# Kernel tuning notes

Measured on AMD Instinct MI355X. Metric: run time of the kernel, lower is better.

The kernel has to match this reference:

```python
import jax, jax.numpy as jnp
import numpy as np

L, N, E, H = 2048, 4, 2048, 16
D = E // H  # head_dim = 128
SCALE = D ** -0.5
NEG = -10000.0


def setup_inputs() -> dict:
    key = jax.random.key(0)
    ks = jax.random.split(key, 10)
    s = 0.02
    return {
        "query": jax.random.normal(ks[0], (L, N, E), jnp.float32),
        "key": jax.random.normal(ks[1], (L, N, E), jnp.float32),
        "wq": jax.random.normal(ks[2], (E, E), jnp.float32) * s,
        "wq_bias": jax.random.normal(ks[3], (E,), jnp.float32) * s,
        "wk": jax.random.normal(ks[4], (E, E), jnp.float32) * s,
        "wk_bias": jax.random.normal(ks[5], (E,), jnp.float32) * s,
        "wv": jax.random.normal(ks[6], (E, E), jnp.float32) * s,
        "wv_bias": jax.random.normal(ks[7], (E,), jnp.float32) * s,
        "wout": jax.random.normal(ks[8], (E, E), jnp.float32) * s,
        "wout_bias": jax.random.normal(ks[9], (E,), jnp.float32) * s,
    }


def reference(query, key, wq, wq_bias, wk, wk_bias, wv, wv_bias, wout, wout_bias):
    # query/key: (L, N, E). Projections: y = x @ W^T + b  (W: [inner, E])
    q = query @ wq.T + wq_bias          # (L, N, E)
    k = key @ wk.T + wk_bias
    v = key @ wv.T + wv_bias
    # split heads -> (N, H, L, D)
    def split(x):
        return x.reshape(L, N, H, D).transpose(1, 2, 0, 3)
    q, k, v = split(q) * SCALE, split(k), split(v)
    # scores (N, H, L, L) with causal mask (tril), fill -10000 like torch code
    attn = jnp.einsum("nhqd,nhkd->nhqk", q, k)
    causal = jnp.tril(jnp.ones((L, L), dtype=bool))
    attn = jnp.where(causal[None, None], attn, NEG)
    attn = jax.nn.softmax(attn, axis=-1)
    out = jnp.einsum("nhqk,nhkd->nhqd", attn, v)  # (N, H, L, D)
    out = out.transpose(2, 0, 1, 3).reshape(L, N, E)
    return out @ wout.T + wout_bias
```

## Files before the change

kernel.cpp:

```cpp
#include <hip/hip_runtime.h>
#include <hip/hip_bf16.h>
#include <cstdint>
#include <cstddef>

typedef __attribute__((ext_vector_type(8))) short short8;
typedef __attribute__((ext_vector_type(4))) float float4v;

#define L_SEQ 2048
#define N_B   4
#define E_DIM 2048
#define N_H   16
#define H_D   128
#define C1_SCALE_LOG2E 0.12751744f

static __device__ __forceinline__ unsigned short f2bf(float f) {
  union { float f; unsigned int u; } x; x.f = f;
  unsigned int u = x.u;
  u = u + 0x7fffu + ((u >> 16) & 1u);
  return (unsigned short)(u >> 16);
}

static __device__ __forceinline__ void g2l16(const void* g, void* l) {
  __builtin_amdgcn_global_load_lds(
      (const __attribute__((address_space(1))) unsigned int*)g,
      (__attribute__((address_space(3))) unsigned int*)l, 16, 0, 0);
}

__global__ __launch_bounds__(256) void cvt_kernel(const float* __restrict__ in,
                                                  unsigned short* __restrict__ out,
                                                  int n8) {
  int i = blockIdx.x * blockDim.x + threadIdx.x;
  if (i >= n8) return;
  const float4* p = (const float4*)in;
  float4 a = p[2 * i];
  float4 b = p[2 * i + 1];
  short8 o;
  o[0] = (short)f2bf(a.x); o[1] = (short)f2bf(a.y);
  o[2] = (short)f2bf(a.z); o[3] = (short)f2bf(a.w);
  o[4] = (short)f2bf(b.x); o[5] = (short)f2bf(b.y);
  o[6] = (short)f2bf(b.z); o[7] = (short)f2bf(b.w);
  *(short8*)(out + 8 * (size_t)i) = o;
}

template <int MODE>
__global__ __launch_bounds__(256) void gemm_bt(const unsigned short* __restrict__ A,
                                               const unsigned short* __restrict__ B,
                                               const float* __restrict__ bias,
                                               void* __restrict__ Cout) {
  __shared__ unsigned short sA[128 * 32];
  __shared__ unsigned short sB[128 * 32];
  const int tid = threadIdx.x;
  const int wv = tid >> 6, ln = tid & 63;
  const int wr = wv >> 1, wc = wv & 1;
  const int lhi = ln >> 4, llo = ln & 15;
  const int kr = lhi * 8;
  const int m0 = blockIdx.y * 128, n0 = blockIdx.x * 128;

  float4v acc[4][4] = {};

  const char* Ab = (const char*)A;
  const char* Bb = (const char*)B;
  const int srow = wv * 16 + (ln >> 2);
  const int scb  = (ln & 3) * 16;

  for (int k0 = 0; k0 < E_DIM; k0 += 32) {
#pragma unroll
    for (int c = 0; c < 2; ++c) {
      g2l16(Ab + ((size_t)(m0 + c * 64 + srow) * E_DIM + k0) * 2 + scb,
            (char*)sA + c * 4096 + wv * 1024);
      g2l16(Bb + ((size_t)(n0 + c * 64 + srow) * E_DIM + k0) * 2 + scb,
            (char*)sB + c * 4096 + wv * 1024);
    }
    __syncthreads();
    short8 af[4], bfr[4];
#pragma unroll
    for (int i = 0; i < 4; ++i)
      af[i] = *(const short8*)(sA + (wr * 64 + i * 16 + llo) * 32 + kr);
#pragma unroll
    for (int jx = 0; jx < 4; ++jx)
      bfr[jx] = *(const short8*)(sB + (wc * 64 + jx * 16 + llo) * 32 + kr);
#pragma unroll
    for (int i = 0; i < 4; ++i)
#pragma unroll
      for (int jx = 0; jx < 4; ++jx)
        acc[i][jx] = __builtin_amdgcn_mfma_f32_16x16x32_bf16(af[i], bfr[jx], acc[i][jx], 0, 0, 0);
    __syncthreads();
  }

  float bcol[4];
#pragma unroll
  for (int jx = 0; jx < 4; ++jx) bcol[jx] = bias[n0 + wc * 64 + jx * 16 + llo];

#pragma unroll
  for (int i = 0; i < 4; ++i) {
#pragma unroll
    for (int r = 0; r < 4; ++r) {
      const int m = m0 + wr * 64 + i * 16 + lhi * 4 + r;
      const int l = m >> 2, nb = m & 3;
#pragma unroll
      for (int jx = 0; jx < 4; ++jx) {
        const int cN = n0 + wc * 64 + jx * 16 + llo;
        const float v = acc[i][jx][r] + bcol[jx];
        if (MODE == 0) {
          ((float*)Cout)[(size_t)m * E_DIM + cN] = v;
        } else if (MODE == 1) {
          const int h = cN >> 7, d = cN & 127;
          ((unsigned short*)Cout)[(((size_t)(nb * N_H + h)) * L_SEQ + l) * H_D + d] = f2bf(v);
        } else {
          const int h = cN >> 7, d = cN & 127;
          ((unsigned short*)Cout)[(((size_t)(nb * N_H + h)) * H_D + d) * L_SEQ + l] = f2bf(v);
        }
      }
    }
  }
}

__global__ __launch_bounds__(512, 2) void flash_attn(const unsigned short* __restrict__ Q,
                                                     const unsigned short* __restrict__ K,
                                                     const unsigned short* __restrict__ VT,
                                                     unsigned short* __restrict__ Cc) {
  __shared__ unsigned short sK[128 * 128];
  __shared__ unsigned short sV[128 * 128];
  const int tid = threadIdx.x;
  const int wv = tid >> 6, ln = tid & 63;
  const int lhi = ln >> 4, llo = ln & 15;
  const int kr = lhi * 8;
  const int lin = (int)blockIdx.x;
  const int xcd = lin & 7, slot = lin >> 3;
  const int hgrp = slot >> 4, pos = slot & 15;
  const int tq = (hgrp & 1) ? (15 - pos) : pos;
  const int nh = hgrp * 8 + xcd;
  const size_t hoff = (size_t)nh * (L_SEQ * H_D);
  const unsigned short* Qp = Q + hoff;
  const char* Kb = (const char*)(K + hoff);
  const char* Vb = (const char*)(VT + hoff);

  short8 qf[4];
#pragma unroll
  for (int kk = 0; kk < 4; ++kk)
    qf[kk] = *(const short8*)(Qp + (size_t)(tq * 128 + wv * 16 + llo) * H_D + kk * 32 + kr);

  float4v o_acc[8] = {};
  float mst[4], lst[4];
#pragma unroll
  for (int r = 0; r < 4; ++r) { mst[r] = -1e30f; lst[r] = 0.f; }

  for (int j = 0; j <= tq; ++j) {
#pragma unroll
    for (int t = 0; t < 4; ++t) {
      const int row = wv * 16 + t * 4 + lhi;
      const int sc = llo ^ (row & 7);
      g2l16(Kb + ((size_t)(j * 128 + row) * H_D) * 2 + sc * 16,
            (char*)sK + wv * 4096 + t * 1024);
      g2l16(Vb + ((size_t)row * L_SEQ + j * 128) * 2 + sc * 16,
            (char*)sV + wv * 4096 + t * 1024);
    }
    __syncthreads();

    float4v s[8] = {};
#pragma unroll
    for (int kk = 0; kk < 4; ++kk) {
      const int u0 = kk * 4 + lhi;
#pragma unroll
      for (int jj = 0; jj < 8; ++jj) {
        const int row = jj * 16 + llo;
        const short8 b = *(const short8*)(sK + row * 128 + (u0 ^ (row & 7)) * 8);
        s[jj] = __builtin_amdgcn_mfma_f32_16x16x32_bf16(qf[kk], b, s[jj], 0, 0, 0);
      }
    }

#pragma unroll
    for (int jj = 0; jj < 8; ++jj)
#pragma unroll
      for (int r = 0; r < 4; ++r)
        s[jj][r] *= C1_SCALE_LOG2E;
    const bool diag = (j == tq);
    if (diag) {
      const int qrow = wv * 16 + lhi * 4;
#pragma unroll
      for (int jj = 0; jj < 8; ++jj) {
        const int c = jj * 16 + llo;
#pragma unroll
        for (int r = 0; r < 4; ++r)
          if (c > qrow + r) s[jj][r] = -1e30f;
      }
    }

    float alpha[4];
#pragma unroll
    for (int r = 0; r < 4; ++r) {
      float rm = fmaxf(fmaxf(fmaxf(s[0][r], s[1][r]), fmaxf(s[2][r], s[3][r])),
                       fmaxf(fmaxf(s[4][r], s[5][r]), fmaxf(s[6][r], s[7][r])));
      rm = fmaxf(rm, __shfl_xor(rm, 1, 64));
      rm = fmaxf(rm, __shfl_xor(rm, 2, 64));
      rm = fmaxf(rm, __shfl_xor(rm, 4, 64));
      rm = fmaxf(rm, __shfl_xor(rm, 8, 64));
      const float mnew = fmaxf(mst[r], rm);
      const float a = __builtin_exp2f(mst[r] - mnew);
      mst[r] = mnew;
      alpha[r] = a;
      float rs = 0.f;
#pragma unroll
      for (int jj = 0; jj < 8; ++jj) {
        const float pv = __builtin_exp2f(s[jj][r] - mnew);
        s[jj][r] = pv;
        rs += pv;
      }
      rs += __shfl_xor(rs, 1, 64);
      rs += __shfl_xor(rs, 2, 64);
      rs += __shfl_xor(rs, 4, 64);
      rs += __shfl_xor(rs, 8, 64);
      lst[r] = lst[r] * a + rs;
    }

    __syncthreads();

#pragma unroll
    for (int r = 0; r < 4; ++r) {
      const int rl = wv * 16 + lhi * 4 + r;
#pragma unroll
      for (int jj = 0; jj < 8; ++jj) {
        const int c = jj * 16 + llo;
        const float v = s[jj][r];
        const float v2 = __shfl_xor(v, 1, 64);
        if ((llo & 1) == 0) {
          const unsigned int pk = (unsigned int)f2bf(v) | ((unsigned int)f2bf(v2) << 16);
          const int u = ((c >> 3) ^ (rl & 7));
          *(unsigned int*)(sK + rl * 128 + u * 8 + (c & 7)) = pk;
        }
      }
    }

#pragma unroll
    for (int jj = 0; jj < 8; ++jj) {
      float4v t = o_acc[jj];
      t[0] *= alpha[0]; t[1] *= alpha[1];
      t[2] *= alpha[2]; t[3] *= alpha[3];
      o_acc[jj] = t;
    }
#pragma unroll
    for (int kk = 0; kk < 4; ++kk) {
      const int u0 = kk * 4 + lhi;
      const int rowp = wv * 16 + llo;
      const short8 a = *(const short8*)(sK + rowp * 128 + (u0 ^ (rowp & 7)) * 8);
#pragma unroll
      for (int jj = 0; jj < 8; ++jj) {
        const int row = jj * 16 + llo;
        const short8 b = *(const short8*)(sV + row * 128 + (u0 ^ (row & 7)) * 8);
        o_acc[jj] = __builtin_amdgcn_mfma_f32_16x16x32_bf16(a, b, o_acc[jj], 0, 0, 0);
      }
    }
    __syncthreads();
  }

  const int nb = nh >> 4, h = nh & 15;
#pragma unroll
  for (int r = 0; r < 4; ++r) {
    const float inv = 1.0f / lst[r];
    const int rl = wv * 16 + lhi * 4 + r;
#pragma unroll
    for (int jj = 0; jj < 8; ++jj) {
      const int c = jj * 16 + llo;
      const float v = o_acc[jj][r] * inv;
      const float v2 = __shfl_xor(v, 1, 64);
      if ((llo & 1) == 0) {
        const unsigned int pk = (unsigned int)f2bf(v) | ((unsigned int)f2bf(v2) << 16);
        *(unsigned int*)(sK + rl * 128 + c) = pk;
      }
    }
  }
  __syncthreads();
#pragma unroll
  for (int t = 0; t < 4; ++t) {
    const int row = wv * 16 + t * 4 + lhi;
    const short8 val = *(const short8*)(sK + row * 128 + llo * 8);
    const int qg = tq * 128 + row;
    *(short8*)(Cc + ((size_t)qg * N_B + nb) * E_DIM + h * H_D + llo * 8) = val;
  }
}

extern "C" void kernel_launch(void* const* d_in, const int* in_sizes, int n_in,
                              void* d_out, int out_size, void* d_ws, size_t ws_size,
                              hipStream_t stream) {
  (void)in_sizes; (void)n_in; (void)out_size; (void)ws_size;
  const float* query = (const float*)d_in[0];
  const float* key   = (const float*)d_in[1];
  const float* wq = (const float*)d_in[2];
  const float* bq = (const float*)d_in[3];
  const float* wk = (const float*)d_in[4];
  const float* bk = (const float*)d_in[5];
  const float* wv = (const float*)d_in[6];
  const float* bv = (const float*)d_in[7];
  const float* wo = (const float*)d_in[8];
  const float* bo = (const float*)d_in[9];

  char* ws = (char*)d_ws;
  unsigned short* Xq = (unsigned short*)(ws);
  unsigned short* Xk = (unsigned short*)(ws + 33554432);
  unsigned short* Wq = (unsigned short*)(ws + 67108864);
  unsigned short* Wk = (unsigned short*)(ws + 75497472);
  unsigned short* Wv = (unsigned short*)(ws + 83886080);
  unsigned short* Wo = (unsigned short*)(ws + 92274688);
  unsigned short* Qh = (unsigned short*)(ws + 100663296);
  unsigned short* Kh = (unsigned short*)(ws + 134217728);
  unsigned short* VT = (unsigned short*)(ws + 167772160);
  unsigned short* Cc = Xq;

  const int nAct8 = L_SEQ * N_B * E_DIM / 8;
  const int nW8   = E_DIM * E_DIM / 8;
  cvt_kernel<<<dim3((nAct8 + 255) / 256), 256, 0, stream>>>(query, Xq, nAct8);
  cvt_kernel<<<dim3((nAct8 + 255) / 256), 256, 0, stream>>>(key, Xk, nAct8);
  cvt_kernel<<<dim3((nW8 + 255) / 256), 256, 0, stream>>>(wq, Wq, nW8);
  cvt_kernel<<<dim3((nW8 + 255) / 256), 256, 0, stream>>>(wk, Wk, nW8);
  cvt_kernel<<<dim3((nW8 + 255) / 256), 256, 0, stream>>>(wv, Wv, nW8);
  cvt_kernel<<<dim3((nW8 + 255) / 256), 256, 0, stream>>>(wo, Wo, nW8);

  dim3 gg(E_DIM / 128, (L_SEQ * N_B) / 128);
  gemm_bt<1><<<gg, 256, 0, stream>>>(Xq, Wq, bq, Qh);
  gemm_bt<1><<<gg, 256, 0, stream>>>(Xk, Wk, bk, Kh);
  gemm_bt<2><<<gg, 256, 0, stream>>>(Xk, Wv, bv, VT);

  flash_attn<<<dim3(N_B * N_H * (L_SEQ / 128)), 512, 0, stream>>>(Qh, Kh, VT, Cc);

  gemm_bt<0><<<gg, 256, 0, stream>>>(Cc, Wo, bo, d_out);
}
```

Measured before the change: 897.7 us.

## Replace projection GEMMs with 256x256 tiled, double-buffered, XCD-aware pipelined kernel

Replaces the 128x128 single-buffered projection GEMM with a 256x256 tile kernel of 8 waves. It double-buffers LDS with a 64-wide K step, swizzles LDS columns to avoid bank conflicts, interleaves global-to-LDS prefetch with MFMA phases under explicit barriers and s_setprio, and maps blocks to XCDs so M panels stay local. The goal is to raise MFMA utilisation and data reuse and to hide load latency in the four GEMMs. In exchange it uses more LDS and registers and a fragile hand-tuned waitcnt schedule, and it runs only 256 blocks.

New measurement: 811.9 us. -9.6%, faster.

```diff
diff --git a/kernel.cpp b/kernel.cpp
--- a/kernel.cpp
+++ b/kernel.cpp
@@ -42,65 +42,155 @@
   *(short8*)(out + 8 * (size_t)i) = o;
 }
 
+#define BAR2()                                         \
+  do {                                                 \
+    __builtin_amdgcn_s_barrier();                      \
+    asm volatile("" ::: "memory");                     \
+    __builtin_amdgcn_sched_barrier(0);                 \
+  } while (0)
+
+#define LGKM0() asm volatile("s_waitcnt lgkmcnt(0)" ::: "memory")
+
+#define STAGE(MAT, KT, KS, SLOT)                                          \
+  do {                                                                    \
+    g2l16((MAT) + (size_t)soff[0] + (size_t)((KT) * 128 + (KS) * 64),     \
+          (char*)lds + (SLOT) * 16384 + lbase[0]);                        \
+    g2l16((MAT) + (size_t)soff[1] + (size_t)((KT) * 128 + (KS) * 64),     \
+          (char*)lds + (SLOT) * 16384 + lbase[1]);                        \
+  } while (0)
+
 template <int MODE>
-__global__ __launch_bounds__(256) void gemm_bt(const unsigned short* __restrict__ A,
+__global__ __launch_bounds__(512) void gemm256(const unsigned short* __restrict__ A,
                                                const unsigned short* __restrict__ B,
                                                const float* __restrict__ bias,
                                                void* __restrict__ Cout) {
-  __shared__ unsigned short sA[128 * 32];
-  __shared__ unsigned short sB[128 * 32];
+  __shared__ unsigned short lds[8][8192];
   const int tid = threadIdx.x;
-  const int wv = tid >> 6, ln = tid & 63;
-  const int wr = wv >> 1, wc = wv & 1;
+  const int wid = tid >> 6, ln = tid & 63;
+  const int wm = wid >> 2, wn = wid & 3;
   const int lhi = ln >> 4, llo = ln & 15;
-  const int kr = lhi * 8;
-  const int m0 = blockIdx.y * 128, n0 = blockIdx.x * 128;
-
-  float4v acc[4][4] = {};
-
-  const char* Ab = (const char*)A;
-  const char* Bb = (const char*)B;
-  const int srow = wv * 16 + (ln >> 2);
-  const int scb  = (ln & 3) * 16;
-
-  for (int k0 = 0; k0 < E_DIM; k0 += 32) {
-#pragma unroll
-    for (int c = 0; c < 2; ++c) {
-      g2l16(Ab + ((size_t)(m0 + c * 64 + srow) * E_DIM + k0) * 2 + scb,
-            (char*)sA + c * 4096 + wv * 1024);
-      g2l16(Bb + ((size_t)(n0 + c * 64 + srow) * E_DIM + k0) * 2 + scb,
-            (char*)sB + c * 4096 + wv * 1024);
-    }
-    __syncthreads();
-    short8 af[4], bfr[4];
-#pragma unroll
-    for (int i = 0; i < 4; ++i)
-      af[i] = *(const short8*)(sA + (wr * 64 + i * 16 + llo) * 32 + kr);
-#pragma unroll
-    for (int jx = 0; jx < 4; ++jx)
-      bfr[jx] = *(const short8*)(sB + (wc * 64 + jx * 16 + llo) * 32 + kr);
-#pragma unroll
-    for (int i = 0; i < 4; ++i)
-#pragma unroll
-      for (int jx = 0; jx < 4; ++jx)
-        acc[i][jx] = __builtin_amdgcn_mfma_f32_16x16x32_bf16(af[i], bfr[jx], acc[i][jx], 0, 0, 0);
-    __syncthreads();
+
+  const int lin = (int)blockIdx.x;
+  const int xcd = lin & 7, sl = lin >> 3;
+  const int n0 = (sl & 7) * 256;
+  const int m0 = (xcd * 4 + (sl >> 3)) * 256;
+
+  const char* Apan = (const char*)(A + (size_t)m0 * E_DIM);
+  const char* Bpan = (const char*)(B + (size_t)n0 * E_DIM);
+
+  int soff[2], lbase[2];
+#pragma unroll
+  for (int i = 0; i < 2; ++i) {
+    const int g = i * 512 + wid * 64 + ln;
+    const int row = g >> 2, c = g & 3;
+    soff[i] = row * (E_DIM * 2) + ((c ^ (row & 3)) << 4);
+    lbase[i] = (i * 512 + wid * 64) * 16;
+  }
+
+  float4v acc[8][4] = {};
+  const int arow = wm * 128 + llo;
+  const int brow = wn * 64 + llo;
+  const int swz = (lhi ^ (llo & 3)) * 8;
+  constexpr int NT = E_DIM / 64;
+
+  STAGE(Apan, 0, 0, 0); STAGE(Apan, 0, 1, 1);
+  STAGE(Bpan, 0, 0, 2); STAGE(Bpan, 0, 1, 3);
+  STAGE(Bpan, 1, 0, 6); STAGE(Apan, 1, 0, 4); STAGE(Bpan, 1, 1, 7);
+  asm volatile("s_waitcnt vmcnt(6)" ::: "memory");
+  BAR2();
+
+  short8 av[4], bv[4];
+  for (int kt = 0; kt < NT; ++kt) {
+    const int bb = kt & 1, ob = bb ^ 1;
+    const unsigned short* pA = lds[bb * 4 + 0];
+    const unsigned short* pB = lds[bb * 4 + 2];
+
+#pragma unroll
+    for (int mr = 0; mr < 4; ++mr)
+      av[mr] = *(const short8*)(pA + (arow + mr * 16) * 32 + swz);
+#pragma unroll
+    for (int nr = 0; nr < 4; ++nr)
+      bv[nr] = *(const short8*)(pB + (brow + nr * 16) * 32 + swz);
+    if (kt + 1 < NT) STAGE(Apan, kt + 1, 1, ob * 4 + 1);
+    __builtin_amdgcn_s_barrier();
+    LGKM0();
+    __builtin_amdgcn_s_setprio(1);
+#pragma unroll
+    for (int mr = 0; mr < 4; ++mr)
+#pragma unroll
+      for (int nr = 0; nr < 4; ++nr)
+        acc[mr][nr] = __builtin_amdgcn_mfma_f32_16x16x32_bf16(av[mr], bv[nr], acc[mr][nr], 0, 0, 0);
+    __builtin_amdgcn_s_setprio(0);
+    BAR2();
+
+#pragma unroll
+    for (int mr = 0; mr < 4; ++mr)
+      av[mr] = *(const short8*)(pA + (arow + 64 + mr * 16) * 32 + swz);
+    if (kt + 2 < NT) STAGE(Bpan, kt + 2, 0, bb * 4 + 2);
+    __builtin_amdgcn_s_barrier();
+    LGKM0();
+    __builtin_amdgcn_s_setprio(1);
+#pragma unroll
+    for (int mr = 0; mr < 4; ++mr)
+#pragma unroll
+      for (int nr = 0; nr < 4; ++nr)
+        acc[4 + mr][nr] = __builtin_amdgcn_mfma_f32_16x16x32_bf16(av[mr], bv[nr], acc[4 + mr][nr], 0, 0, 0);
+    __builtin_amdgcn_s_setprio(0);
+    BAR2();
+
+#pragma unroll
+    for (int mr = 0; mr < 4; ++mr)
+      av[mr] = *(const short8*)(pA + 8192 + (arow + mr * 16) * 32 + swz);
+#pragma unroll
+    for (int nr = 0; nr < 4; ++nr)
+      bv[nr] = *(const short8*)(pB + 8192 + (brow + nr * 16) * 32 + swz);
+    if (kt + 2 < NT) STAGE(Apan, kt + 2, 0, bb * 4 + 0);
+    __builtin_amdgcn_s_barrier();
+    LGKM0();
+    __builtin_amdgcn_s_setprio(1);
+#pragma unroll
+    for (int mr = 0; mr < 4; ++mr)
+#pragma unroll
+      for (int nr = 0; nr < 4; ++nr)
+        acc[mr][nr] = __builtin_amdgcn_mfma_f32_16x16x32_bf16(av[mr], bv[nr], acc[mr][nr], 0, 0, 0);
+    __builtin_amdgcn_s_setprio(0);
+    BAR2();
+
+#pragma unroll
+    for (int mr = 0; mr < 4; ++mr)
+      av[mr] = *(const short8*)(pA + 8192 + (arow + 64 + mr * 16) * 32 + swz);
+    if (kt + 2 < NT) STAGE(Bpan, kt + 2, 1, bb * 4 + 3);
+    __builtin_amdgcn_s_barrier();
+    LGKM0();
+    __builtin_amdgcn_s_setprio(1);
+#pragma unroll
+    for (int mr = 0; mr < 4; ++mr)
+#pragma unroll
+      for (int nr = 0; nr < 4; ++nr)
+        acc[4 + mr][nr] = __builtin_amdgcn_mfma_f32_16x16x32_bf16(av[mr], bv[nr], acc[4 + mr][nr], 0, 0, 0);
+    __builtin_amdgcn_s_setprio(0);
+
+    if (kt < NT - 1) {
+      if (kt == NT - 2) { asm volatile("s_waitcnt vmcnt(0)" ::: "memory"); }
+      else              { asm volatile("s_waitcnt vmcnt(6)" ::: "memory"); }
+      BAR2();
+    }
   }
 
   float bcol[4];
 #pragma unroll
-  for (int jx = 0; jx < 4; ++jx) bcol[jx] = bias[n0 + wc * 64 + jx * 16 + llo];
-
-#pragma unroll
-  for (int i = 0; i < 4; ++i) {
+  for (int nr = 0; nr < 4; ++nr) bcol[nr] = bias[n0 + wn * 64 + nr * 16 + llo];
+
+#pragma unroll
+  for (int mr = 0; mr < 8; ++mr) {
 #pragma unroll
     for (int r = 0; r < 4; ++r) {
-      const int m = m0 + wr * 64 + i * 16 + lhi * 4 + r;
+      const int m = m0 + wm * 128 + mr * 16 + lhi * 4 + r;
       const int l = m >> 2, nb = m & 3;
 #pragma unroll
-      for (int jx = 0; jx < 4; ++jx) {
-        const int cN = n0 + wc * 64 + jx * 16 + llo;
-        const float v = acc[i][jx][r] + bcol[jx];
+      for (int nr = 0; nr < 4; ++nr) {
+        const int cN = n0 + wn * 64 + nr * 16 + llo;
+        const float v = acc[mr][nr][r] + bcol[nr];
         if (MODE == 0) {
           ((float*)Cout)[(size_t)m * E_DIM + cN] = v;
         } else if (MODE == 1) {
@@ -315,12 +405,12 @@
   cvt_kernel<<<dim3((nW8 + 255) / 256), 256, 0, stream>>>(wv, Wv, nW8);
   cvt_kernel<<<dim3((nW8 + 255) / 256), 256, 0, stream>>>(wo, Wo, nW8);
 
-  dim3 gg(E_DIM / 128, (L_SEQ * N_B) / 128);
-  gemm_bt<1><<<gg, 256, 0, stream>>>(Xq, Wq, bq, Qh);
-  gemm_bt<1><<<gg, 256, 0, stream>>>(Xk, Wk, bk, Kh);
-  gemm_bt<2><<<gg, 256, 0, stream>>>(Xk, Wv, bv, VT);
+  dim3 gg(256);
+  gemm256<1><<<gg, 512, 0, stream>>>(Xq, Wq, bq, Qh);
+  gemm256<1><<<gg, 512, 0, stream>>>(Xk, Wk, bk, Kh);
+  gemm256<2><<<gg, 512, 0, stream>>>(Xk, Wv, bv, VT);
 
   flash_attn<<<dim3(N_B * N_H * (L_SEQ / 128)), 512, 0, stream>>>(Qh, Kh, VT, Cc);
 
-  gemm_bt<0><<<gg, 256, 0, stream>>>(Cc, Wo, bo, d_out);
-}
+  gemm256<0><<<gg, 512, 0, stream>>>(Cc, Wo, bo, d_out);
+}
```
